# Optimization experiments

Hardware: AMD Instinct MI355X
Metric: run time of the kernel (lower is better)

Reference implementation:

```python
import jax, jax.numpy as jnp
import numpy as np

CUTOFFS = (2000, 20000, 50000)  # shortlist end, tail cluster boundaries; last == vocab
B, H, V = 8192, 1024, 50000
N_TAIL = len(CUTOFFS) - 1  # 2


def setup_inputs() -> dict:
    key = jax.random.key(0)
    ks = jax.random.split(key, 10)
    hidden = jax.random.normal(ks[0], (B, H), jnp.float32)
    targets = jax.random.randint(ks[1], (B,), 0, V, dtype=jnp.int64)
    embed_weight = jax.random.normal(ks[2], (V, H), jnp.float32) * 0.02
    # head: tail_vectors = nn.Linear(H, n_tail) -> W:(n_tail,H), b:(n_tail,)
    tail_vec_W = jax.random.normal(ks[3], (N_TAIL, H), jnp.float32) * 0.02
    tail_vec_b = jax.random.normal(ks[4], (N_TAIL,), jnp.float32) * 0.02
    shortlist_bias = jax.random.normal(ks[5], (CUTOFFS[0],), jnp.float32)
    bias0 = jax.random.normal(ks[6], (CUTOFFS[1] - CUTOFFS[0],), jnp.float32)
    bias1 = jax.random.normal(ks[7], (CUTOFFS[2] - CUTOFFS[1],), jnp.float32)
    # down_i = nn.Linear(H, H // 4**i, bias=False) -> W:(H//4**i, H)
    down0_W = jax.random.normal(ks[8], (H, H), jnp.float32) * (1.0 / np.sqrt(H))
    down1_W = jax.random.normal(ks[9], (H // 4, H), jnp.float32) * (1.0 / np.sqrt(H))
    return {
        "hidden": hidden, "embed_weight": embed_weight,
        "tail_vec_W": tail_vec_W, "tail_vec_b": tail_vec_b,
        "shortlist_bias": shortlist_bias, "bias0": bias0, "bias1": bias1,
        "down0_W": down0_W, "down1_W": down1_W, "targets": targets,
    }


def _cluster_ids(targets):
    # data-dependent sizes -> host-side index computation (matches torch nonzero)
    t = np.asarray(targets)
    ids = []
    for i in range(N_TAIL):
        ids.append(jnp.asarray(np.nonzero((t >= CUTOFFS[i]) & (t < CUTOFFS[i + 1]))[0]))
    return ids


def reference(hidden, embed_weight, tail_vec_W, tail_vec_b, shortlist_bias,
              bias0, bias1, down0_W, down1_W, targets):
    idx0, idx1 = _cluster_ids(targets)
    # head: shortlist logits + one logit per tail cluster
    shortlist = embed_weight[:CUTOFFS[0]]                       # (c0, H)
    head = jnp.concatenate(
        [hidden @ shortlist.T + shortlist_bias[None, :],         # (B, c0)
         hidden @ tail_vec_W.T + tail_vec_b[None, :]], axis=1)   # (B, n_tail)
    # tail cluster 0: down0 is H->H (reduce_factor**0 == 1, still applied)
    dec0 = embed_weight[CUTOFFS[0]:CUTOFFS[1]] @ down0_W.T       # (18000, H)
    out0 = (hidden[idx0] @ down0_W.T) @ dec0.T + bias0[None, :]  # (n0, 18000)
    # tail cluster 1: down1 is H -> H//4
    dec1 = embed_weight[CUTOFFS[1]:CUTOFFS[2]] @ down1_W.T       # (30000, 256)
    out1 = (hidden[idx1] @ down1_W.T) @ dec1.T + bias1[None, :]  # (n1, 30000)
    return (head, out0, out1)
```

## Files before the change

### kernel.cpp

```cpp
#include <hip/hip_runtime.h>
#include <hip/hip_bf16.h>

#define CUT0 2000
#define CUT1 20000
#define CUT2 50000
#define BSZ  8192
#define HDIM 1024
#define N0MAX 18000
#define N1MAX 30000
#define HEADW 2002

typedef __attribute__((ext_vector_type(8))) short bf16x8;
typedef __attribute__((ext_vector_type(4))) float f32x4;
typedef __attribute__((ext_vector_type(4))) unsigned short us4;

__device__ __forceinline__ unsigned short f2bf(float x) {
    unsigned u = __float_as_uint(x);
    unsigned r = u + 0x7fffu + ((u >> 16) & 1u);
    return (unsigned short)(r >> 16);
}

__device__ __forceinline__ bf16x8 pack8(f32x4 a, f32x4 b) {
    bf16x8 w;
    w[0] = (short)f2bf(a[0]); w[1] = (short)f2bf(a[1]);
    w[2] = (short)f2bf(a[2]); w[3] = (short)f2bf(a[3]);
    w[4] = (short)f2bf(b[0]); w[5] = (short)f2bf(b[1]);
    w[6] = (short)f2bf(b[2]); w[7] = (short)f2bf(b[3]);
    return w;
}

typedef const __attribute__((address_space(1))) void* gas_ptr;
typedef __attribute__((address_space(3))) void* las_ptr;

__device__ __forceinline__ void load_lds16(const void* g, void* l) {
    __builtin_amdgcn_global_load_lds((gas_ptr)g, (las_ptr)l, 16, 0, 0);
}

__global__ __launch_bounds__(1024) void build_idx(const int* __restrict__ targets,
                                                  int* __restrict__ n0,
                                                  int* __restrict__ n1,
                                                  int* __restrict__ idx0,
                                                  int* __restrict__ idx1) {
    __shared__ int s0[1024], s1[1024];
    const int t = threadIdx.x;
    const int base = t * 8;
    int tg[8];
    int c0 = 0, c1 = 0;
#pragma unroll
    for (int i = 0; i < 8; ++i) {
        tg[i] = targets[base + i];
        c0 += (tg[i] >= CUT0 && tg[i] < CUT1) ? 1 : 0;
        c1 += (tg[i] >= CUT1) ? 1 : 0;
    }
    s0[t] = c0; s1[t] = c1;
    __syncthreads();
    for (int off = 1; off < 1024; off <<= 1) {
        int v0 = 0, v1 = 0;
        if (t >= off) { v0 = s0[t - off]; v1 = s1[t - off]; }
        __syncthreads();
        s0[t] += v0; s1[t] += v1;
        __syncthreads();
    }
    int p0 = s0[t] - c0, p1 = s1[t] - c1;
#pragma unroll
    for (int i = 0; i < 8; ++i) {
        if (tg[i] >= CUT0 && tg[i] < CUT1)      idx0[p0++] = base + i;
        else if (tg[i] >= CUT1)                 idx1[p1++] = base + i;
    }
    if (t == 1023) { *n0 = s0[1023]; *n1 = s1[1023]; }
}

__global__ __launch_bounds__(256) void cvt_bf16(const float* __restrict__ src,
                                                unsigned short* __restrict__ dst,
                                                long long n) {
    long long i = ((long long)blockIdx.x * 256 + threadIdx.x) * 8;
    const long long stride = (long long)gridDim.x * 256 * 8;
    for (; i < n; i += stride) {
        f32x4 a = *(const f32x4*)(src + i);
        f32x4 b = *(const f32x4*)(src + i + 4);
        us4 p = { f2bf(a[0]), f2bf(a[1]), f2bf(a[2]), f2bf(a[3]) };
        us4 q = { f2bf(b[0]), f2bf(b[1]), f2bf(b[2]), f2bf(b[3]) };
        *(us4*)(dst + i)     = p;
        *(us4*)(dst + i + 4) = q;
    }
}

__global__ __launch_bounds__(256) void tail_head(const float* __restrict__ hidden,
                                                 const float* __restrict__ tailW,
                                                 const float* __restrict__ tailb,
                                                 float* __restrict__ out) {
    const int wave = threadIdx.x >> 6, lane = threadIdx.x & 63;
    const int row = blockIdx.x * 4 + wave;
    const float* h = hidden + (long long)row * HDIM;
    float s0 = 0.f, s1 = 0.f;
    for (int k = lane; k < HDIM; k += 64) {
        float x = h[k];
        s0 += x * tailW[k];
        s1 += x * tailW[HDIM + k];
    }
#pragma unroll
    for (int off = 32; off; off >>= 1) {
        s0 += __shfl_down(s0, off);
        s1 += __shfl_down(s1, off);
    }
    if (lane == 0) {
        out[(long long)row * HEADW + CUT0]     = s0 + tailb[0];
        out[(long long)row * HEADW + CUT0 + 1] = s1 + tailb[1];
    }
}

template<bool A_F32, bool SPLIT_GATHER, bool OUT_BF16, bool HAS_BIAS>
__global__ __launch_bounds__(512) void gemm256(
    const void* __restrict__ Av, const float* __restrict__ AgF,
    const unsigned short* __restrict__ B,
    int gsplit, int gbase, const int* __restrict__ idxTail,
    int Mbase, const int* __restrict__ Mdev,
    int N, int K,
    const float* __restrict__ bias,
    void* __restrict__ Cv,
    long long coff, const int* __restrict__ coffM, long long coffScale,
    int ldC)
{
    const int M = Mbase + (Mdev ? *Mdev : 0);
    const int m0 = blockIdx.y * 256;
    const int n0 = blockIdx.x * 256;
    if (m0 >= M) return;

    __shared__ unsigned short As[4][8192];
    __shared__ unsigned short Bs[4][8192];

    const int tid  = threadIdx.x;
    const int wave = tid >> 6, lane = tid & 63;
    const int wr = wave >> 2;
    const int wc = wave & 3;
    const int lrow = lane & 15;
    const int quad = lane >> 4;

    const int srow = lane >> 2;
    const int scol = (((lane & 3) ^ ((srow >> 1) & 3)) << 3);
    int tr0 = wave * 32 + srow, tr1 = tr0 + 16;
    int bn0 = n0 + tr0; bn0 = bn0 < N ? bn0 : N - 1;
    int bn1 = n0 + tr1; bn1 = bn1 < N ? bn1 : N - 1;
    const unsigned short* bP0 = B + (long long)bn0 * K + scol;
    const unsigned short* bP1 = B + (long long)bn1 * K + scol;

    const unsigned short* aP0 = nullptr;
    const unsigned short* aP1 = nullptr;
    const float* aF = nullptr;
    int oA0 = 0, oA1 = 0, sA0 = 0, sA1 = 0;
    if constexpr (!A_F32) {
        int am0 = m0 + tr0; am0 = am0 < M ? am0 : M - 1;
        int am1 = m0 + tr1; am1 = am1 < M ? am1 : M - 1;
        long long ar0, ar1;
        if constexpr (SPLIT_GATHER) {
            ar0 = (am0 < gsplit) ? (long long)(gbase + am0) : (long long)idxTail[am0 - gsplit];
            ar1 = (am1 < gsplit) ? (long long)(gbase + am1) : (long long)idxTail[am1 - gsplit];
        } else { ar0 = am0; ar1 = am1; }
        const unsigned short* Ab = (const unsigned short*)Av;
        aP0 = Ab + ar0 * (long long)K + scol;
        aP1 = Ab + ar1 * (long long)K + scol;
    } else {
        const int rA  = lane >> 1;
        const int trA = wave * 32 + rA;
        int amF = m0 + trA; amF = amF < M ? amF : M - 1;
        long long rowi; const float* bp;
        if constexpr (SPLIT_GATHER) {
            if (amF < gsplit) { rowi = (long long)(gbase + amF); bp = (const float*)Av; }
            else              { rowi = (long long)idxTail[amF - gsplit]; bp = AgF; }
        } else { rowi = amF; bp = (const float*)Av; }
        aF  = bp + rowi * (long long)K;
        sA0 = (lane & 1);
        sA1 = 2 + (lane & 1);
        const int xA = (rA >> 1) & 3;
        oA0 = trA * 32 + ((sA0 ^ xA) << 3);
        oA1 = trA * 32 + ((sA1 ^ xA) << 3);
    }

    f32x4 acc[8][4];
#pragma unroll
    for (int i = 0; i < 8; ++i)
#pragma unroll
        for (int j = 0; j < 4; ++j) acc[i][j] = (f32x4){0.f, 0.f, 0.f, 0.f};

    const int KT = K >> 5;

    auto issueB = [&](int tt) {
        unsigned short* bs = &Bs[tt & 3][wave * 1024];
        load_lds16(bP0 + (tt << 5), bs);
        load_lds16(bP1 + (tt << 5), bs + 512);
    };
    auto issueA16 = [&](int tt) {
        unsigned short* as = &As[tt & 3][wave * 1024];
        load_lds16(aP0 + (tt << 5), as);
        load_lds16(aP1 + (tt << 5), as + 512);
    };

    const int npro = KT < 3 ? KT : 3;
    for (int tt = 0; tt < npro; ++tt) {
        issueB(tt);
        if constexpr (!A_F32) {
            issueA16(tt);
        } else {
            const float* p = aF + (tt << 5);
            f32x4 x0 = *(const f32x4*)(p + sA0 * 8);
            f32x4 x1 = *(const f32x4*)(p + sA0 * 8 + 4);
            f32x4 y0 = *(const f32x4*)(p + sA1 * 8);
            f32x4 y1 = *(const f32x4*)(p + sA1 * 8 + 4);
            *(bf16x8*)&As[tt & 3][oA0] = pack8(x0, x1);
            *(bf16x8*)&As[tt & 3][oA1] = pack8(y0, y1);
        }
    }
    if constexpr (A_F32)
        asm volatile("s_waitcnt lgkmcnt(0)" ::: "memory");

    const int rdswz = ((quad ^ ((lrow >> 1) & 3)) << 3);

    for (int t = 0; t < KT; ++t) {
        const int tt = t + 3;
        const bool pf = (tt < KT);

        f32x4 x0, x1, y0, y1;
        if constexpr (!A_F32) {
            if (pf) { issueB(tt); issueA16(tt); }
        } else {
            if (pf) {
                issueB(tt);
                const float* p = aF + (tt << 5);
                x0 = *(const f32x4*)(p + sA0 * 8);
                x1 = *(const f32x4*)(p + sA0 * 8 + 4);
                y0 = *(const f32x4*)(p + sA1 * 8);
                y1 = *(const f32x4*)(p + sA1 * 8 + 4);
            }
        }

        int infl = KT - 1 - t; if (infl > 3) infl = 3;
        if constexpr (!A_F32) {
            if (infl >= 3)      asm volatile("s_waitcnt vmcnt(12)" ::: "memory");
            else if (infl == 2) asm volatile("s_waitcnt vmcnt(8)"  ::: "memory");
            else if (infl == 1) asm volatile("s_waitcnt vmcnt(4)"  ::: "memory");
            else                asm volatile("s_waitcnt vmcnt(0)"  ::: "memory");
        } else {
            if (infl >= 3)      asm volatile("s_waitcnt vmcnt(10)" ::: "memory");
            else if (infl == 2) asm volatile("s_waitcnt vmcnt(4)"  ::: "memory");
            else if (infl == 1) asm volatile("s_waitcnt vmcnt(2)"  ::: "memory");
            else                asm volatile("s_waitcnt vmcnt(0)"  ::: "memory");
        }

        __builtin_amdgcn_s_barrier();
        asm volatile("" ::: "memory");

        const unsigned short* Asl = &As[t & 3][0];
        const unsigned short* Bsl = &Bs[t & 3][0];

        bf16x8 a[8], b[4];
#pragma unroll
        for (int mi = 0; mi < 8; ++mi) {
            const int R = wr * 128 + mi * 16 + lrow;
            a[mi] = *(const bf16x8*)&Asl[R * 32 + rdswz];
        }
#pragma unroll
        for (int nj = 0; nj < 4; ++nj) {
            const int R = wc * 64 + nj * 16 + lrow;
            b[nj] = *(const bf16x8*)&Bsl[R * 32 + rdswz];
        }

        __builtin_amdgcn_s_setprio(1);
#pragma unroll
        for (int mi = 0; mi < 8; ++mi)
#pragma unroll
            for (int nj = 0; nj < 4; ++nj)
                acc[mi][nj] = __builtin_amdgcn_mfma_f32_16x16x32_bf16(
                    a[mi], b[nj], acc[mi][nj], 0, 0, 0);
        __builtin_amdgcn_s_setprio(0);

        if constexpr (A_F32) {
            if (pf) {
                *(bf16x8*)&As[tt & 3][oA0] = pack8(x0, x1);
                *(bf16x8*)&As[tt & 3][oA1] = pack8(y0, y1);
            }
            asm volatile("s_waitcnt lgkmcnt(0)" ::: "memory");
        }

        asm volatile("" ::: "memory");
        __builtin_amdgcn_s_barrier();
    }

    long long cbase = coff + (coffM ? (long long)(*coffM) * coffScale : 0ll);
#pragma unroll
    for (int mi = 0; mi < 8; ++mi) {
#pragma unroll
        for (int v = 0; v < 4; ++v) {
            int m = m0 + wr * 128 + mi * 16 + quad * 4 + v;
            if (m >= M) continue;
#pragma unroll
            for (int nj = 0; nj < 4; ++nj) {
                int n = n0 + wc * 64 + nj * 16 + lrow;
                if (n >= N) continue;
                float r = acc[mi][nj][v];
                if constexpr (OUT_BF16) {
                    ((unsigned short*)Cv)[(long long)m * ldC + n] = f2bf(r);
                } else {
                    if constexpr (HAS_BIAS) r += bias[n];
                    ((float*)Cv)[cbase + (long long)m * ldC + n] = r;
                }
            }
        }
    }
}

extern "C" void kernel_launch(void* const* d_in, const int* in_sizes, int n_in,
                              void* d_out, int out_size, void* d_ws, size_t ws_size,
                              hipStream_t stream) {
    (void)in_sizes; (void)n_in; (void)out_size; (void)ws_size;
    const float* hidden  = (const float*)d_in[0];
    const float* embed   = (const float*)d_in[1];
    const float* tailW   = (const float*)d_in[2];
    const float* tailb   = (const float*)d_in[3];
    const float* slbias  = (const float*)d_in[4];
    const float* bias0   = (const float*)d_in[5];
    const float* bias1   = (const float*)d_in[6];
    const float* down0   = (const float*)d_in[7];
    const float* down1   = (const float*)d_in[8];
    const int*   targets = (const int*)d_in[9];
    float* out = (float*)d_out;

    char* ws = (char*)d_ws;
    int* n0p  = (int*)ws;
    int* n1p  = n0p + 1;
    int* idx0 = (int*)(ws + 256);
    int* idx1 = idx0 + BSZ;
    size_t off = 256 + 2 * (size_t)BSZ * 4;
    unsigned short* hbf  = (unsigned short*)(ws + off); off += (size_t)BSZ * HDIM * 2;
    unsigned short* ebf  = (unsigned short*)(ws + off); off += (size_t)CUT0 * HDIM * 2;
    unsigned short* c0   = (unsigned short*)(ws + off);
    off += (size_t)(N0MAX + BSZ) * HDIM * 2;
    unsigned short* c1   = (unsigned short*)(ws + off);
    off += (size_t)(N1MAX + BSZ) * 256 * 2;
    unsigned short* d0bf = (unsigned short*)(ws + off); off += (size_t)HDIM * HDIM * 2;
    unsigned short* d1bf = (unsigned short*)(ws + off); off += (size_t)256 * HDIM * 2;

    build_idx<<<1, 1024, 0, stream>>>(targets, n0p, n1p, idx0, idx1);

    cvt_bf16<<<2048, 256, 0, stream>>>(hidden, hbf, (long long)BSZ * HDIM);
    cvt_bf16<<<512,  256, 0, stream>>>(embed,  ebf, (long long)CUT0 * HDIM);
    cvt_bf16<<<512,  256, 0, stream>>>(down0, d0bf, (long long)HDIM * HDIM);
    cvt_bf16<<<128,  256, 0, stream>>>(down1, d1bf, (long long)256 * HDIM);

    gemm256<false, false, false, true><<<dim3(8, 32), 512, 0, stream>>>(
        hbf, nullptr, ebf, 0, 0, nullptr,
        BSZ, nullptr, CUT0, HDIM,
        slbias, out, 0ll, nullptr, 0ll, HEADW);

    tail_head<<<BSZ / 4, 256, 0, stream>>>(hidden, tailW, tailb, out);

    gemm256<true, true, true, false><<<dim3(4, 103), 512, 0, stream>>>(
        embed, hidden, d0bf, N0MAX, CUT0, idx0,
        N0MAX, n0p, HDIM, HDIM,
        nullptr, c0, 0ll, nullptr, 0ll, HDIM);

    gemm256<true, true, true, false><<<dim3(1, 150), 512, 0, stream>>>(
        embed, hidden, d1bf, N1MAX, CUT1, idx1,
        N1MAX, n1p, 256, HDIM,
        nullptr, c1, 0ll, nullptr, 0ll, 256);

    gemm256<false, false, false, true><<<dim3(71, 32), 512, 0, stream>>>(
        c0 + (size_t)N0MAX * HDIM, nullptr, c0, 0, 0, nullptr,
        0, n0p, N0MAX, HDIM,
        bias0, out, (long long)BSZ * HEADW, nullptr, 0ll, N0MAX);

    gemm256<false, false, false, true><<<dim3(118, 32), 512, 0, stream>>>(
        c1 + (size_t)N1MAX * 256, nullptr, c1, 0, 0, nullptr,
        0, n1p, N1MAX, 256,
        bias1, out, (long long)BSZ * HEADW, n0p, (long long)N0MAX, N1MAX);
}
```

Baseline: 1.648 ms.

## Merge conversions and group GEMM launches, fold tail logits into head GEMM

Replaces the four separate bf16 conversion kernels with one block-dispatched conversion kernel that also converts the tail-vector weights and builds a combined bias. This lets the head GEMM cover all 2002 columns and drops the scalar tail_head kernel. The two down-projection GEMMs and the two tail-output GEMMs are each merged into one grouped launch that picks its operands by block index. The aim is to cut launch count and idle tails between small kernels, at the cost of extra branching and more unevenly sized work per grid.

```diff
diff --git a/kernel.cpp b/kernel.cpp
--- a/kernel.cpp
+++ b/kernel.cpp
@@ -70,62 +70,47 @@
     if (t == 1023) { *n0 = s0[1023]; *n1 = s1[1023]; }
 }
 
-__global__ __launch_bounds__(256) void cvt_bf16(const float* __restrict__ src,
-                                                unsigned short* __restrict__ dst,
-                                                long long n) {
-    long long i = ((long long)blockIdx.x * 256 + threadIdx.x) * 8;
-    const long long stride = (long long)gridDim.x * 256 * 8;
-    for (; i < n; i += stride) {
-        f32x4 a = *(const f32x4*)(src + i);
-        f32x4 b = *(const f32x4*)(src + i + 4);
-        us4 p = { f2bf(a[0]), f2bf(a[1]), f2bf(a[2]), f2bf(a[3]) };
-        us4 q = { f2bf(b[0]), f2bf(b[1]), f2bf(b[2]), f2bf(b[3]) };
-        *(us4*)(dst + i)     = p;
-        *(us4*)(dst + i + 4) = q;
-    }
-}
-
-__global__ __launch_bounds__(256) void tail_head(const float* __restrict__ hidden,
-                                                 const float* __restrict__ tailW,
-                                                 const float* __restrict__ tailb,
-                                                 float* __restrict__ out) {
-    const int wave = threadIdx.x >> 6, lane = threadIdx.x & 63;
-    const int row = blockIdx.x * 4 + wave;
-    const float* h = hidden + (long long)row * HDIM;
-    float s0 = 0.f, s1 = 0.f;
-    for (int k = lane; k < HDIM; k += 64) {
-        float x = h[k];
-        s0 += x * tailW[k];
-        s1 += x * tailW[HDIM + k];
-    }
-#pragma unroll
-    for (int off = 32; off; off >>= 1) {
-        s0 += __shfl_down(s0, off);
-        s1 += __shfl_down(s1, off);
-    }
-    if (lane == 0) {
-        out[(long long)row * HEADW + CUT0]     = s0 + tailb[0];
-        out[(long long)row * HEADW + CUT0 + 1] = s1 + tailb[1];
-    }
+#define CVT_TOTAL 5738
+__global__ __launch_bounds__(256) void cvt_all(
+    const float* __restrict__ hidden, const float* __restrict__ embed,
+    const float* __restrict__ tailW,  const float* __restrict__ down0,
+    const float* __restrict__ down1,  const float* __restrict__ slbias,
+    const float* __restrict__ tailb,
+    unsigned short* __restrict__ hbf, unsigned short* __restrict__ ebf,
+    unsigned short* __restrict__ d0bf, unsigned short* __restrict__ d1bf,
+    float* __restrict__ bias2002)
+{
+    const int b = blockIdx.x;
+    const float* src; unsigned short* dst; long long e;
+    if (b < 4096)      { src = hidden; dst = hbf;  e = (long long)b * 2048; }
+    else if (b < 5096) { src = embed;  dst = ebf;  e = (long long)(b - 4096) * 2048; }
+    else if (b == 5096){ src = tailW;  dst = ebf + (size_t)CUT0 * HDIM; e = 0; }
+    else if (b < 5609) { src = down0;  dst = d0bf; e = (long long)(b - 5097) * 2048; }
+    else if (b < 5737) { src = down1;  dst = d1bf; e = (long long)(b - 5609) * 2048; }
+    else {
+        for (int j = threadIdx.x; j < HEADW; j += 256)
+            bias2002[j] = (j < CUT0) ? slbias[j] : tailb[j - CUT0];
+        return;
+    }
+    const long long i = e + (long long)threadIdx.x * 8;
+    f32x4 a = *(const f32x4*)(src + i);
+    f32x4 c = *(const f32x4*)(src + i + 4);
+    us4 p = { f2bf(a[0]), f2bf(a[1]), f2bf(a[2]), f2bf(a[3]) };
+    us4 q = { f2bf(c[0]), f2bf(c[1]), f2bf(c[2]), f2bf(c[3]) };
+    *(us4*)(dst + i)     = p;
+    *(us4*)(dst + i + 4) = q;
 }
 
 template<bool A_F32, bool SPLIT_GATHER, bool OUT_BF16, bool HAS_BIAS>
-__global__ __launch_bounds__(512) void gemm256(
+__device__ __forceinline__ void gemm_body(
     const void* __restrict__ Av, const float* __restrict__ AgF,
     const unsigned short* __restrict__ B,
     int gsplit, int gbase, const int* __restrict__ idxTail,
-    int Mbase, const int* __restrict__ Mdev,
-    int N, int K,
+    int M, int N, int K,
     const float* __restrict__ bias,
-    void* __restrict__ Cv,
-    long long coff, const int* __restrict__ coffM, long long coffScale,
-    int ldC)
+    void* __restrict__ Cv, long long cbase, int ldC,
+    int m0, int n0)
 {
-    const int M = Mbase + (Mdev ? *Mdev : 0);
-    const int m0 = blockIdx.y * 256;
-    const int n0 = blockIdx.x * 256;
-    if (m0 >= M) return;
-
     __shared__ unsigned short As[4][8192];
     __shared__ unsigned short Bs[4][8192];
 
@@ -285,7 +270,6 @@
         __builtin_amdgcn_s_barrier();
     }
 
-    long long cbase = coff + (coffM ? (long long)(*coffM) * coffScale : 0ll);
 #pragma unroll
     for (int mi = 0; mi < 8; ++mi) {
 #pragma unroll
@@ -306,6 +290,69 @@
             }
         }
     }
+}
+
+__global__ __launch_bounds__(512) void gemm_head(
+    const unsigned short* __restrict__ hbf, const unsigned short* __restrict__ ebf,
+    const float* __restrict__ bias2002, float* __restrict__ out)
+{
+    gemm_body<false, false, false, true>(
+        hbf, nullptr, ebf, 0, 0, nullptr,
+        BSZ, HEADW, HDIM, bias2002, out, 0ll, HEADW,
+        (int)blockIdx.y * 256, (int)blockIdx.x * 256);
+}
+
+__global__ __launch_bounds__(512) void gemm_c0c1(
+    const float* __restrict__ embed, const float* __restrict__ hidden,
+    const unsigned short* __restrict__ d0bf, const unsigned short* __restrict__ d1bf,
+    const int* __restrict__ idx0, const int* __restrict__ idx1,
+    const int* __restrict__ n0p, const int* __restrict__ n1p,
+    unsigned short* __restrict__ c0, unsigned short* __restrict__ c1)
+{
+    int bx = blockIdx.x;
+    const unsigned short* Bb; const int* idxT;
+    int gsplit, gbase, M, N, ldC; unsigned short* C;
+    if (bx < 4) {
+        Bb = d0bf; idxT = idx0; gsplit = N0MAX; gbase = CUT0;
+        M = N0MAX + *n0p; N = HDIM; ldC = HDIM; C = c0;
+    } else {
+        bx -= 4;
+        Bb = d1bf; idxT = idx1; gsplit = N1MAX; gbase = CUT1;
+        M = N1MAX + *n1p; N = 256; ldC = 256; C = c1;
+    }
+    const int m0 = (int)blockIdx.y * 256;
+    const int n0 = bx * 256;
+    if (m0 >= M) return;
+    gemm_body<true, true, true, false>(
+        embed, hidden, Bb, gsplit, gbase, idxT,
+        M, N, HDIM, nullptr, C, 0ll, ldC, m0, n0);
+}
+
+__global__ __launch_bounds__(512) void gemm_out01(
+    const unsigned short* __restrict__ c0, const unsigned short* __restrict__ c1,
+    const int* __restrict__ n0p, const int* __restrict__ n1p,
+    const float* __restrict__ bias0, const float* __restrict__ bias1,
+    float* __restrict__ out)
+{
+    int bx = blockIdx.x;
+    const unsigned short *A, *B; const float* bias;
+    int M, N, K, ldC; long long cbase;
+    if (bx < 71) {
+        A = c0 + (size_t)N0MAX * HDIM; B = c0; bias = bias0;
+        M = *n0p; N = N0MAX; K = HDIM; ldC = N0MAX;
+        cbase = (long long)BSZ * HEADW;
+    } else {
+        bx -= 71;
+        A = c1 + (size_t)N1MAX * 256; B = c1; bias = bias1;
+        M = *n1p; N = N1MAX; K = 256; ldC = N1MAX;
+        cbase = (long long)BSZ * HEADW + (long long)(*n0p) * N0MAX;
+    }
+    const int m0 = (int)blockIdx.y * 256;
+    const int n0 = bx * 256;
+    if (m0 >= M) return;
+    gemm_body<false, false, false, true>(
+        A, nullptr, B, 0, 0, nullptr,
+        M, N, K, bias, out, cbase, ldC, m0, n0);
 }
 
 extern "C" void kernel_launch(void* const* d_in, const int* in_sizes, int n_in,
@@ -331,7 +378,8 @@
     int* idx1 = idx0 + BSZ;
     size_t off = 256 + 2 * (size_t)BSZ * 4;
     unsigned short* hbf  = (unsigned short*)(ws + off); off += (size_t)BSZ * HDIM * 2;
-    unsigned short* ebf  = (unsigned short*)(ws + off); off += (size_t)CUT0 * HDIM * 2;
+    unsigned short* ebf  = (unsigned short*)(ws + off); off += (size_t)HEADW * HDIM * 2;
+    float* bias2002      = (float*)(ws + off);          off += 2048 * 4;
     unsigned short* c0   = (unsigned short*)(ws + off);
     off += (size_t)(N0MAX + BSZ) * HDIM * 2;
     unsigned short* c1   = (unsigned short*)(ws + off);
@@ -341,35 +389,15 @@
 
     build_idx<<<1, 1024, 0, stream>>>(targets, n0p, n1p, idx0, idx1);
 
-    cvt_bf16<<<2048, 256, 0, stream>>>(hidden, hbf, (long long)BSZ * HDIM);
-    cvt_bf16<<<512,  256, 0, stream>>>(embed,  ebf, (long long)CUT0 * HDIM);
-    cvt_bf16<<<512,  256, 0, stream>>>(down0, d0bf, (long long)HDIM * HDIM);
-    cvt_bf16<<<128,  256, 0, stream>>>(down1, d1bf, (long long)256 * HDIM);
-
-    gemm256<false, false, false, true><<<dim3(8, 32), 512, 0, stream>>>(
-        hbf, nullptr, ebf, 0, 0, nullptr,
-        BSZ, nullptr, CUT0, HDIM,
-        slbias, out, 0ll, nullptr, 0ll, HEADW);
-
-    tail_head<<<BSZ / 4, 256, 0, stream>>>(hidden, tailW, tailb, out);
-
-    gemm256<true, true, true, false><<<dim3(4, 103), 512, 0, stream>>>(
-        embed, hidden, d0bf, N0MAX, CUT0, idx0,
-        N0MAX, n0p, HDIM, HDIM,
-        nullptr, c0, 0ll, nullptr, 0ll, HDIM);
-
-    gemm256<true, true, true, false><<<dim3(1, 150), 512, 0, stream>>>(
-        embed, hidden, d1bf, N1MAX, CUT1, idx1,
-        N1MAX, n1p, 256, HDIM,
-        nullptr, c1, 0ll, nullptr, 0ll, 256);
-
-    gemm256<false, false, false, true><<<dim3(71, 32), 512, 0, stream>>>(
-        c0 + (size_t)N0MAX * HDIM, nullptr, c0, 0, 0, nullptr,
-        0, n0p, N0MAX, HDIM,
-        bias0, out, (long long)BSZ * HEADW, nullptr, 0ll, N0MAX);
-
-    gemm256<false, false, false, true><<<dim3(118, 32), 512, 0, stream>>>(
-        c1 + (size_t)N1MAX * 256, nullptr, c1, 0, 0, nullptr,
-        0, n1p, N1MAX, 256,
-        bias1, out, (long long)BSZ * HEADW, n0p, (long long)N0MAX, N1MAX);
-}
+    cvt_all<<<CVT_TOTAL, 256, 0, stream>>>(
+        hidden, embed, tailW, down0, down1, slbias, tailb,
+        hbf, ebf, d0bf, d1bf, bias2002);
+
+    gemm_c0c1<<<dim3(5, 150), 512, 0, stream>>>(
+        embed, hidden, d0bf, d1bf, idx0, idx1, n0p, n1p, c0, c1);
+
+    gemm_head<<<dim3(8, 32), 512, 0, stream>>>(hbf, ebf, bias2002, out);
+
+    gemm_out01<<<dim3(189, 32), 512, 0, stream>>>(
+        c0, c1, n0p, n1p, bias0, bias1, out);
+}
```

Measured after the change: 1.585 ms. 1.04x faster.
